# Performance work log

Hardware: AMD Instinct MI355X
Metric: run time of the kernel (lower is better)

Reference implementation:

```python
import jax, jax.numpy as jnp
import numpy as np

NUM_HEADS = 16

def setup_inputs() -> dict:
    key = jax.random.key(0)
    ks = jax.random.split(key, 11)
    B, S, D, H = 2, 2048, 1024, 1024
    s = lambda k, shape, scale=1.0: (jax.random.normal(k, shape, dtype=jnp.float32) * scale)
    return {
        "KEY": s(ks[0], (B, S, D)),
        "VALUE": s(ks[1], (B, S, D)),
        "QUERY": s(ks[2], (B, S, D)),
        "Wk_w": s(ks[3], (H, D), 0.02),
        "Wk_b": s(ks[4], (H,), 0.02),
        "Wq_w": s(ks[5], (H, D), 0.02),
        "Wq_b": s(ks[6], (H,), 0.02),
        "Wv_w": s(ks[7], (H, D), 0.02),
        "Wv_b": s(ks[8], (H,), 0.02),
        "Wo_w": s(ks[9], (H, H), 0.02),
        "Wo_b": s(ks[10], (H,), 0.02),
    }


def _split_heads(x, num_heads):
    # torch: reshape (B, S, dh, nh) then permute(0,3,1,2) -> (B, nh, S, dh)
    B, S, H = x.shape
    dh = H // num_heads
    return x.reshape(B, S, dh, num_heads).transpose(0, 3, 1, 2)


def reference(KEY, VALUE, QUERY, Wk_w, Wk_b, Wq_w, Wq_b, Wv_w, Wv_b, Wo_w, Wo_b):
    nh = NUM_HEADS
    k = _split_heads(KEY @ Wk_w.T + Wk_b, nh)      # [B, nh, Sk, dh]
    q = _split_heads(QUERY @ Wq_w.T + Wq_b, nh)    # [B, nh, Sq, dh]
    v = _split_heads(VALUE @ Wv_w.T + Wv_b, nh)    # [B, nh, Sv, dh]
    dh = q.shape[-1]
    score = jnp.einsum('bhij,bhkj->bhik', k, q) / jnp.sqrt(jnp.asarray(dh, k.dtype))  # [B,nh,Sk,Sq]
    # NOTE: faithful to the source — softmax over dim=1 (the HEAD axis)
    attn = jax.nn.softmax(score, axis=1)
    out = jnp.einsum('bhik,bhij->bhjk', attn, v)   # [B, nh, dh, Sq]
    B = out.shape[0]
    # permute(0,2,1,3) -> [B, dh, nh, Sq]; reshape -> [B, dh*nh, Sq]; transpose -> [B, Sq, H]
    out = out.transpose(0, 2, 1, 3).reshape(B, -1, out.shape[-1]).transpose(0, 2, 1)
    res = out @ Wo_w.T + Wo_b                      # dropout is identity in eval mode
    return res
```

## Files before the change

### kernel.cpp

```cpp
#include <hip/hip_runtime.h>
#include <hip/hip_bf16.h>

typedef __attribute__((ext_vector_type(8))) short s8v;
typedef __attribute__((ext_vector_type(4))) short s4v;
typedef __attribute__((ext_vector_type(4))) float f4v;

#define MFMA32(A,B,C) __builtin_amdgcn_mfma_f32_16x16x32_bf16(A,B,C,0,0,0)
#define MFMA16(A,B,C) __builtin_amdgcn_mfma_f32_16x16x16bf16_1k(A,B,C,0,0,0)

typedef __attribute__((address_space(1))) const void* gas1;
typedef __attribute__((address_space(3))) void* las3;
#define GLDS16(g,l) __builtin_amdgcn_global_load_lds((gas1)(const void*)(g),(las3)(void*)(l),16,0,0)

__device__ __forceinline__ unsigned short f2bf(float f){
  unsigned int u = __float_as_uint(f);
  u += 0x7FFFu + ((u>>16)&1u);
  return (unsigned short)(u>>16);
}
__device__ __forceinline__ float bf2f(unsigned short s){
  return __uint_as_float(((unsigned int)s)<<16);
}
__device__ __forceinline__ s4v pack4(f4v v){
  float2 lo; lo.x=v[0]; lo.y=v[1];
  float2 hi; hi.x=v[2]; hi.y=v[3];
  __hip_bfloat162 a = __float22bfloat162_rn(lo);
  __hip_bfloat162 b = __float22bfloat162_rn(hi);
  union{ s4v s; unsigned int u[2]; } r;
  __builtin_memcpy(&r.u[0], &a, 4);
  __builtin_memcpy(&r.u[1], &b, 4);
  return r.s;
}

#define EXPC 0.18033688011112042f

#define BARRIER() do{                                        \
  asm volatile("s_waitcnt lgkmcnt(0)" ::: "memory");         \
  __builtin_amdgcn_s_barrier();                              \
  asm volatile("" ::: "memory");                             \
}while(0)

__global__ __launch_bounds__(256) void conv_in(
    const float* __restrict__ KEY, const float* __restrict__ QUERY, const float* __restrict__ VALUE,
    const float* __restrict__ Wk, const float* __restrict__ Wq, const float* __restrict__ Wv,
    unsigned short* __restrict__ kb, unsigned short* __restrict__ qb,
    unsigned short* __restrict__ vb, unsigned short* __restrict__ wkb,
    unsigned short* __restrict__ wqb, unsigned short* __restrict__ wvb)
{
  const int z = blockIdx.y;
  const size_t n = (z<3)? (size_t)4194304 : (size_t)1048576;
  size_t idx = ((size_t)blockIdx.x*256 + threadIdx.x)*8;
  if(idx >= n) return;
  const float* s = (z==0)?KEY:(z==1)?QUERY:(z==2)?VALUE:(z==3)?Wk:(z==4)?Wq:Wv;
  unsigned short* d = (z==0)?kb:(z==1)?qb:(z==2)?vb:(z==3)?wkb:(z==4)?wqb:wvb;
  float4 a = *(const float4*)&s[idx];
  float4 b = *(const float4*)&s[idx+4];
  union{ s8v v; s4v h[2]; } r;
  r.h[0]=pack4((f4v){a.x,a.y,a.z,a.w});
  r.h[1]=pack4((f4v){b.x,b.y,b.z,b.w});
  *(s8v*)&d[idx]=r.v;
}

__global__ void pack_wo(const float* __restrict__ wo, unsigned short* __restrict__ wop){
  int idx = blockIdx.x*256 + threadIdx.x;
  if(idx >= 1024*1024) return;
  int o = idx >> 10, r = idx & 1023, h = r >> 6, j = r & 63;
  wop[idx] = f2bf(wo[o*1024 + j*16 + h]);
}

__global__ __launch_bounds__(256) void proj_gemm(
    const unsigned short* __restrict__ kbp, const unsigned short* __restrict__ qbp,
    const unsigned short* __restrict__ vbp,
    const unsigned short* __restrict__ wkb, const unsigned short* __restrict__ wqb,
    const unsigned short* __restrict__ wvb,
    const float* __restrict__ bk, const float* __restrict__ bq, const float* __restrict__ bv,
    unsigned short* __restrict__ kh, unsigned short* __restrict__ qh,
    unsigned short* __restrict__ vt)
{
  __shared__ short As[128*64];
  __shared__ short Bs[128*64];
  const int t = threadIdx.x;
  const int z = blockIdx.z;
  const unsigned short* A; const unsigned short* W; const float* bias;
  if(z==0){A=kbp; W=wkb; bias=bk;}
  else if(z==1){A=qbp; W=wqb; bias=bq;}
  else {A=vbp; W=wvb; bias=bv;}
  const int m0 = blockIdx.x*128, n0 = blockIdx.y*128;
  const int l = t&63, w = t>>6;
  const int wm = (w>>1)*64, wn = (w&1)*64;
  const int row16 = l&15, quad = l>>4;
  f4v acc[4][4];
  #pragma unroll
  for(int i=0;i<4;i++)
    #pragma unroll
    for(int j=0;j<4;j++) acc[i][j] = (f4v){0.f,0.f,0.f,0.f};

  const int sr=t>>3, sc=(t&7)*8;
  for(int k0=0;k0<1024;k0+=64){
    #pragma unroll
    for(int p=0;p<4;p++){
      GLDS16(&A[(size_t)(m0+p*32+sr)*1024 + k0 + sc], &As[(p*32+sr)*64 + sc]);
      GLDS16(&W[(size_t)(n0+p*32+sr)*1024 + k0 + sc], &Bs[(p*32+sr)*64 + sc]);
    }
    __syncthreads();
    #pragma unroll
    for(int kk=0; kk<64; kk+=32){
      s8v af[4], bf[4];
      #pragma unroll
      for(int mt=0;mt<4;mt++) af[mt] = *(const s8v*)&As[(wm+mt*16+row16)*64 + kk + quad*8];
      #pragma unroll
      for(int nt=0;nt<4;nt++) bf[nt] = *(const s8v*)&Bs[(wn+nt*16+row16)*64 + kk + quad*8];
      #pragma unroll
      for(int mt=0;mt<4;mt++)
        #pragma unroll
        for(int nt=0;nt<4;nt++)
          acc[mt][nt] = MFMA32(af[mt], bf[nt], acc[mt][nt]);
    }
    __syncthreads();
  }

  const int jb = (n0+wn)>>4;
  const float bv0 = bias[n0+wn+ 0+row16];
  const float bv1 = bias[n0+wn+16+row16];
  const float bv2 = bias[n0+wn+32+row16];
  const float bv3 = bias[n0+wn+48+row16];
  if(z==2){
    #pragma unroll
    for(int mt=0;mt<4;mt++){
      const int m = m0+wm+mt*16;
      const int bb=m>>11, ss=m&2047, it=ss>>4;
      const size_t base = (((size_t)(bb*16+row16))*128 + it)*64;
      #pragma unroll
      for(int nt=0;nt<4;nt++){
        const float bn = (nt==0)?bv0:(nt==1)?bv1:(nt==2)?bv2:bv3;
        f4v vals = {acc[mt][nt][0]+bn, acc[mt][nt][1]+bn,
                    acc[mt][nt][2]+bn, acc[mt][nt][3]+bn};
        *(s4v*)&vt[(base + jb+nt)*16 + quad*4] = pack4(vals);
      }
    }
  } else {
    unsigned short* dst = (z==0)? kh : qh;
    #pragma unroll
    for(int mt=0;mt<4;mt++){
      #pragma unroll
      for(int r=0;r<4;r++){
        const int m = m0+wm+mt*16+quad*4+r;
        const int bb=m>>11, ss=m&2047;
        f4v vals = {acc[mt][0][r]+bv0, acc[mt][1][r]+bv1,
                    acc[mt][2][r]+bv2, acc[mt][3][r]+bv3};
        *(s4v*)&dst[((size_t)(bb*16+row16)*2048 + ss)*64 + jb] = pack4(vals);
      }
    }
  }
}

__global__ __launch_bounds__(512) void fused_attn(
    const unsigned short* __restrict__ kh, const unsigned short* __restrict__ qh,
    const unsigned short* __restrict__ vt, unsigned short* __restrict__ opart)
{
  __shared__ unsigned short Ks[256*64];
  __shared__ unsigned short Vs[1024*16];
  __shared__ f4v dpart[2][4][64];

  const int t=threadIdx.x, l=t&63, w=t>>6;
  const int qg=w>>2, hg=w&3;
  const int row16=l&15, quad=l>>4;
  const int bid=blockIdx.x;
  const int combo=bid&7, qb=bid>>3;
  const int ih=combo&3, b=combo>>2;
  const int q0=qb*32+qg*16, h0=hg*4;
  const int ibase=ih*512;

  s8v qf[4][2];
  #pragma unroll
  for(int hh=0;hh<4;hh++){
    const unsigned short* qp=&qh[(size_t)((b*16+h0+hh)*2048 + q0+row16)*64];
    qf[hh][0]=*(const s8v*)&qp[quad*8];
    qf[hh][1]=*(const s8v*)&qp[32+quad*8];
  }

  const int ksl=t&7;
  const unsigned short* kp[4]; int kw[4];
  #pragma unroll
  for(int p=0;p<4;p++){
    const int urow=p*64+(t>>3), h=urow>>4, i=urow&15;
    kp[p]=&kh[((size_t)(b*16+h)*2048 + ibase + i)*64 + ksl*8];
    kw[p]=urow*64 + ((ksl^(urow&7))<<3);
  }
  const int half=t&1;
  const int vkey=(t>>3)&3;
  const unsigned short* vp[4]; int vw0[4], vw1[4];
  #pragma unroll
  for(int p=0;p<4;p++){
    const int row=p*256+(t>>1), h=row>>6, j=row&63;
    vp[p]=&vt[((((size_t)(b*16+h))*128 + ih*32)*64 + j)*16 + half*8];
    vw0[p]=row*16 + (((2*half+0)^vkey)<<2);
    vw1[p]=row*16 + (((2*half+1)^vkey)<<2);
  }

  f4v o[4][4];
  #pragma unroll
  for(int i=0;i<4;i++)
    #pragma unroll
    for(int j=0;j<4;j++) o[i][j]=(f4v){0.f,0.f,0.f,0.f};

  s8v kreg[4], vtmp[4];
  #pragma unroll
  for(int p=0;p<4;p++) kreg[p]=*(const s8v*)(kp[p]);
  #pragma unroll
  for(int p=0;p<4;p++) vtmp[p]=*(const s8v*)(vp[p]);
  #pragma unroll
  for(int p=0;p<4;p++) *(s8v*)&Ks[kw[p]] = kreg[p];
  #pragma unroll
  for(int p=0;p<4;p++) kreg[p]=*(const s8v*)(kp[p] + 1024);
  BARRIER();

  const int sw0=(quad^(row16&7))<<3, sw1=((quad+4)^(row16&7))<<3;
  const int vsw=(quad^((row16>>2)&3))<<2;

  #pragma unroll 1
  for(int it=0; it<32; ++it){
    #pragma unroll
    for(int p=0;p<4;p++){
      s4v lo={vtmp[p][0],vtmp[p][1],vtmp[p][2],vtmp[p][3]};
      s4v hi={vtmp[p][4],vtmp[p][5],vtmp[p][6],vtmp[p][7]};
      *(s4v*)&Vs[vw0[p]]=lo;
      *(s4v*)&Vs[vw1[p]]=hi;
    }
    const int tv=((it+1)&31)*1024;
    #pragma unroll
    for(int p=0;p<4;p++) vtmp[p]=*(const s8v*)(vp[p]+tv);
    f4v e0[4];
    #pragma unroll
    for(int hh=0;hh<4;hh++){
      const unsigned short* kb=&Ks[((h0+hh)*16+row16)*64];
      f4v S={0.f,0.f,0.f,0.f};
      S=MFMA32(*(const s8v*)&kb[sw0], qf[hh][0], S);
      S=MFMA32(*(const s8v*)&kb[sw1], qf[hh][1], S);
      #pragma unroll
      for(int r=0;r<4;r++) e0[hh][r]=__builtin_amdgcn_exp2f(S[r]*EXPC);
    }
    f4v d0=(e0[0]+e0[1])+(e0[2]+e0[3]);
    dpart[qg][hg][l]=d0;
    BARRIER();
    f4v s0=(dpart[qg][0][l]+dpart[qg][1][l])+(dpart[qg][2][l]+dpart[qg][3][l]);
    f4v r0;
    #pragma unroll
    for(int r=0;r<4;r++) r0[r]=__builtin_amdgcn_rcpf(s0[r]);
    #pragma unroll
    for(int p=0;p<4;p++) *(s8v*)&Ks[kw[p]] = kreg[p];
    const int tk=((it+2)&31)*1024;
    #pragma unroll
    for(int p=0;p<4;p++) kreg[p]=*(const s8v*)(kp[p]+tk);
    s4v p0[4];
    #pragma unroll
    for(int hh=0;hh<4;hh++) p0[hh]=pack4(e0[hh]*r0);
    #pragma unroll
    for(int hh=0;hh<4;hh++){
      #pragma unroll
      for(int jt=0;jt<4;jt++){
        const int vrow=((h0+hh)*64+jt*16+row16)*16;
        s4v v0=*(const s4v*)&Vs[vrow + vsw];
        o[hh][jt]=MFMA16(v0, p0[hh], o[hh][jt]);
      }
    }
    BARRIER();
  }

  #pragma unroll
  for(int hh=0;hh<4;hh++)
    #pragma unroll
    for(int jt=0;jt<4;jt++)
      *(s4v*)&opart[(size_t)((ih*2+b)*2048 + q0+row16)*1024 + (h0+hh)*64 + jt*16 + quad*4]
        = pack4(o[hh][jt]);
}

__global__ __launch_bounds__(256) void reduce_o(
    const unsigned short* __restrict__ op, unsigned short* __restrict__ out2)
{
  size_t e = ((size_t)blockIdx.x*256 + threadIdx.x)*8;
  s8v a = *(const s8v*)&op[e];
  s8v b = *(const s8v*)&op[(size_t)4194304 + e];
  s8v c = *(const s8v*)&op[(size_t)2*4194304 + e];
  s8v d = *(const s8v*)&op[(size_t)3*4194304 + e];
  f4v lo, hi;
  #pragma unroll
  for(int i=0;i<4;i++)
    lo[i] = (bf2f((unsigned short)a[i])+bf2f((unsigned short)b[i]))
          + (bf2f((unsigned short)c[i])+bf2f((unsigned short)d[i]));
  #pragma unroll
  for(int i=0;i<4;i++)
    hi[i] = (bf2f((unsigned short)a[i+4])+bf2f((unsigned short)b[i+4]))
          + (bf2f((unsigned short)c[i+4])+bf2f((unsigned short)d[i+4]));
  *(s4v*)&out2[e]   = pack4(lo);
  *(s4v*)&out2[e+4] = pack4(hi);
}

__global__ __launch_bounds__(256) void out_gemm(
    const unsigned short* __restrict__ A, const unsigned short* __restrict__ Bm,
    const float* __restrict__ bias, float* __restrict__ out)
{
  __shared__ short As[128*64];
  __shared__ short Bs[128*64];
  const int t=threadIdx.x, l=t&63, w=t>>6;
  const int row16=l&15, quad=l>>4;
  const int m0=blockIdx.x*128, n0=blockIdx.y*128;
  const int wm=(w>>1)*64, wn=(w&1)*64;
  f4v acc[4][4];
  #pragma unroll
  for(int i=0;i<4;i++)
    #pragma unroll
    for(int j=0;j<4;j++) acc[i][j] = (f4v){0.f,0.f,0.f,0.f};

  const int sr=t>>3, sc=(t&7)*8;
  for(int k0=0;k0<1024;k0+=64){
    #pragma unroll
    for(int p=0;p<4;p++){
      GLDS16(&A [(size_t)(m0+p*32+sr)*1024 + k0 + sc], &As[(p*32+sr)*64 + sc]);
      GLDS16(&Bm[(size_t)(n0+p*32+sr)*1024 + k0 + sc], &Bs[(p*32+sr)*64 + sc]);
    }
    __syncthreads();
    #pragma unroll
    for(int kk=0; kk<64; kk+=32){
      s8v af[4], bf[4];
      #pragma unroll
      for(int mt=0;mt<4;mt++) af[mt] = *(const s8v*)&As[(wm+mt*16+row16)*64 + kk + quad*8];
      #pragma unroll
      for(int nt=0;nt<4;nt++) bf[nt] = *(const s8v*)&Bs[(wn+nt*16+row16)*64 + kk + quad*8];
      #pragma unroll
      for(int mt=0;mt<4;mt++)
        #pragma unroll
        for(int nt=0;nt<4;nt++)
          acc[mt][nt] = MFMA32(af[mt], bf[nt], acc[mt][nt]);
    }
    __syncthreads();
  }
  #pragma unroll
  for(int nt=0;nt<4;nt++){
    const int n = n0+wn+nt*16+row16;
    const float bias_n = bias[n];
    #pragma unroll
    for(int mt=0;mt<4;mt++)
      #pragma unroll
      for(int r=0;r<4;r++){
        const int m = m0+wm+mt*16+quad*4+r;
        out[(size_t)m*1024 + n] = acc[mt][nt][r] + bias_n;
      }
  }
}

extern "C" void kernel_launch(void* const* d_in, const int* in_sizes, int n_in,
                              void* d_out, int out_size, void* d_ws, size_t ws_size,
                              hipStream_t stream)
{
  const float* KEY   = (const float*)d_in[0];
  const float* VALUE = (const float*)d_in[1];
  const float* QUERY = (const float*)d_in[2];
  const float* Wk = (const float*)d_in[3];
  const float* bk = (const float*)d_in[4];
  const float* Wq = (const float*)d_in[5];
  const float* bq = (const float*)d_in[6];
  const float* Wv = (const float*)d_in[7];
  const float* bv = (const float*)d_in[8];
  const float* Wo = (const float*)d_in[9];
  const float* bo = (const float*)d_in[10];

  char* ws = (char*)d_ws;
  unsigned short* kb   = (unsigned short*)(ws);
  unsigned short* qb   = (unsigned short*)(ws +  8388608);
  unsigned short* vb   = (unsigned short*)(ws + 16777216);
  unsigned short* wkb  = (unsigned short*)(ws + 25165824);
  unsigned short* wqb  = (unsigned short*)(ws + 27262976);
  unsigned short* wvb  = (unsigned short*)(ws + 29360128);
  unsigned short* kh   = (unsigned short*)(ws + 33554432);
  unsigned short* qh   = (unsigned short*)(ws + 41943040);
  unsigned short* vt   = (unsigned short*)(ws + 50331648);
  unsigned short* opart= (unsigned short*)(ws);
  unsigned short* wop  = (unsigned short*)(ws + 33554432);
  unsigned short* out2 = (unsigned short*)(ws + 35651584);

  conv_in   <<<dim3(2048,6), dim3(256), 0, stream>>>(KEY,QUERY,VALUE,Wk,Wq,Wv,kb,qb,vb,wkb,wqb,wvb);
  proj_gemm <<<dim3(32,8,3), dim3(256), 0, stream>>>(kb,qb,vb,wkb,wqb,wvb,bk,bq,bv,kh,qh,vt);
  fused_attn<<<dim3(512),    dim3(512), 0, stream>>>(kh,qh,vt,opart);
  pack_wo   <<<dim3(4096),   dim3(256), 0, stream>>>(Wo,wop);
  reduce_o  <<<dim3(2048),   dim3(256), 0, stream>>>(opart,out2);
  out_gemm  <<<dim3(32,8),   dim3(256), 0, stream>>>(out2,wop,bo,(float*)d_out);
}
```

Measured before the change: 303.9 us.

## Load attention K/V fragments directly from global and coalesce Wo packing

The fused attention kernel no longer stages K and V tiles through shared memory. Each lane now loads its MFMA operand fragments straight from global memory into registers, prefetching the next K fragment one iteration ahead. The per-iteration trailing barrier is replaced by a double-buffered denominator array, so only one barrier per iteration remains. The pack_wo kernel now reads float4 and transposes through shared memory for vectorized writes, trading cooperative coalesced staging in attention for more, smaller uncoalesced global loads that rely on cache.

```diff
diff --git a/kernel.cpp b/kernel.cpp
--- a/kernel.cpp
+++ b/kernel.cpp
@@ -60,11 +60,24 @@
   *(s8v*)&d[idx]=r.v;
 }
 
-__global__ void pack_wo(const float* __restrict__ wo, unsigned short* __restrict__ wop){
-  int idx = blockIdx.x*256 + threadIdx.x;
-  if(idx >= 1024*1024) return;
-  int o = idx >> 10, r = idx & 1023, h = r >> 6, j = r & 63;
-  wop[idx] = f2bf(wo[o*1024 + j*16 + h]);
+__global__ __launch_bounds__(256) void pack_wo(const float* __restrict__ wo,
+                                              unsigned short* __restrict__ wop){
+  __shared__ unsigned short tile[4][1024];
+  const int o0 = blockIdx.x*4;
+  const int t = threadIdx.x;
+  const int r = t>>6, u = t&63;
+  #pragma unroll
+  for(int e4=0;e4<4;e4++){
+    float4 v = *(const float4*)&wo[(size_t)(o0+r)*1024 + u*16 + e4*4];
+    tile[r][(e4*4+0)*64 + u] = f2bf(v.x);
+    tile[r][(e4*4+1)*64 + u] = f2bf(v.y);
+    tile[r][(e4*4+2)*64 + u] = f2bf(v.z);
+    tile[r][(e4*4+3)*64 + u] = f2bf(v.w);
+  }
+  __syncthreads();
+  const unsigned short* flat = &tile[0][0];
+  *(s8v*)&wop[(size_t)o0*1024 + t*16]     = *(const s8v*)&flat[t*16];
+  *(s8v*)&wop[(size_t)o0*1024 + t*16 + 8] = *(const s8v*)&flat[t*16 + 8];
 }
 
 __global__ __launch_bounds__(256) void proj_gemm(
@@ -157,9 +170,7 @@
     const unsigned short* __restrict__ kh, const unsigned short* __restrict__ qh,
     const unsigned short* __restrict__ vt, unsigned short* __restrict__ opart)
 {
-  __shared__ unsigned short Ks[256*64];
-  __shared__ unsigned short Vs[1024*16];
-  __shared__ f4v dpart[2][4][64];
+  __shared__ f4v dpart[2][2][4][64];
 
   const int t=threadIdx.x, l=t&63, w=t>>6;
   const int qg=w>>2, hg=w&3;
@@ -178,24 +189,8 @@
     qf[hh][1]=*(const s8v*)&qp[32+quad*8];
   }
 
-  const int ksl=t&7;
-  const unsigned short* kp[4]; int kw[4];
-  #pragma unroll
-  for(int p=0;p<4;p++){
-    const int urow=p*64+(t>>3), h=urow>>4, i=urow&15;
-    kp[p]=&kh[((size_t)(b*16+h)*2048 + ibase + i)*64 + ksl*8];
-    kw[p]=urow*64 + ((ksl^(urow&7))<<3);
-  }
-  const int half=t&1;
-  const int vkey=(t>>3)&3;
-  const unsigned short* vp[4]; int vw0[4], vw1[4];
-  #pragma unroll
-  for(int p=0;p<4;p++){
-    const int row=p*256+(t>>1), h=row>>6, j=row&63;
-    vp[p]=&vt[((((size_t)(b*16+h))*128 + ih*32)*64 + j)*16 + half*8];
-    vw0[p]=row*16 + (((2*half+0)^vkey)<<2);
-    vw1[p]=row*16 + (((2*half+1)^vkey)<<2);
-  }
+  const unsigned short* kbase=&kh[((size_t)(b*16+h0)*2048 + ibase + row16)*64 + quad*8];
+  const unsigned short* vbase=&vt[((((size_t)(b*16+h0))*128 + ih*32)*64 + row16)*16 + quad*4];
 
   f4v o[4][4];
   #pragma unroll
@@ -203,67 +198,54 @@
     #pragma unroll
     for(int j=0;j<4;j++) o[i][j]=(f4v){0.f,0.f,0.f,0.f};
 
-  s8v kreg[4], vtmp[4];
-  #pragma unroll
-  for(int p=0;p<4;p++) kreg[p]=*(const s8v*)(kp[p]);
-  #pragma unroll
-  for(int p=0;p<4;p++) vtmp[p]=*(const s8v*)(vp[p]);
-  #pragma unroll
-  for(int p=0;p<4;p++) *(s8v*)&Ks[kw[p]] = kreg[p];
-  #pragma unroll
-  for(int p=0;p<4;p++) kreg[p]=*(const s8v*)(kp[p] + 1024);
-  BARRIER();
-
-  const int sw0=(quad^(row16&7))<<3, sw1=((quad+4)^(row16&7))<<3;
-  const int vsw=(quad^((row16>>2)&3))<<2;
+  s8v kf[4][2];
+  #pragma unroll
+  for(int hh=0;hh<4;hh++){
+    kf[hh][0]=*(const s8v*)(kbase + hh*131072);
+    kf[hh][1]=*(const s8v*)(kbase + hh*131072 + 32);
+  }
 
   #pragma unroll 1
   for(int it=0; it<32; ++it){
-    #pragma unroll
-    for(int p=0;p<4;p++){
-      s4v lo={vtmp[p][0],vtmp[p][1],vtmp[p][2],vtmp[p][3]};
-      s4v hi={vtmp[p][4],vtmp[p][5],vtmp[p][6],vtmp[p][7]};
-      *(s4v*)&Vs[vw0[p]]=lo;
-      *(s4v*)&Vs[vw1[p]]=hi;
-    }
-    const int tv=((it+1)&31)*1024;
-    #pragma unroll
-    for(int p=0;p<4;p++) vtmp[p]=*(const s8v*)(vp[p]+tv);
+    const int par=it&1;
+    const int off=it*1024;
+    s4v vf[4][4];
+    #pragma unroll
+    for(int hh=0;hh<4;hh++)
+      #pragma unroll
+      for(int jt=0;jt<4;jt++)
+        vf[hh][jt]=*(const s4v*)(vbase + off + hh*131072 + jt*256);
     f4v e0[4];
     #pragma unroll
     for(int hh=0;hh<4;hh++){
-      const unsigned short* kb=&Ks[((h0+hh)*16+row16)*64];
       f4v S={0.f,0.f,0.f,0.f};
-      S=MFMA32(*(const s8v*)&kb[sw0], qf[hh][0], S);
-      S=MFMA32(*(const s8v*)&kb[sw1], qf[hh][1], S);
+      S=MFMA32(kf[hh][0], qf[hh][0], S);
+      S=MFMA32(kf[hh][1], qf[hh][1], S);
       #pragma unroll
       for(int r=0;r<4;r++) e0[hh][r]=__builtin_amdgcn_exp2f(S[r]*EXPC);
     }
+    const int offn=((it+1)&31)*1024;
+    #pragma unroll
+    for(int hh=0;hh<4;hh++){
+      kf[hh][0]=*(const s8v*)(kbase + offn + hh*131072);
+      kf[hh][1]=*(const s8v*)(kbase + offn + hh*131072 + 32);
+    }
     f4v d0=(e0[0]+e0[1])+(e0[2]+e0[3]);
-    dpart[qg][hg][l]=d0;
+    dpart[par][qg][hg][l]=d0;
     BARRIER();
-    f4v s0=(dpart[qg][0][l]+dpart[qg][1][l])+(dpart[qg][2][l]+dpart[qg][3][l]);
+    f4v s0=(dpart[par][qg][0][l]+dpart[par][qg][1][l])
+          +(dpart[par][qg][2][l]+dpart[par][qg][3][l]);
     f4v r0;
     #pragma unroll
     for(int r=0;r<4;r++) r0[r]=__builtin_amdgcn_rcpf(s0[r]);
-    #pragma unroll
-    for(int p=0;p<4;p++) *(s8v*)&Ks[kw[p]] = kreg[p];
-    const int tk=((it+2)&31)*1024;
-    #pragma unroll
-    for(int p=0;p<4;p++) kreg[p]=*(const s8v*)(kp[p]+tk);
     s4v p0[4];
     #pragma unroll
     for(int hh=0;hh<4;hh++) p0[hh]=pack4(e0[hh]*r0);
     #pragma unroll
-    for(int hh=0;hh<4;hh++){
-      #pragma unroll
-      for(int jt=0;jt<4;jt++){
-        const int vrow=((h0+hh)*64+jt*16+row16)*16;
-        s4v v0=*(const s4v*)&Vs[vrow + vsw];
-        o[hh][jt]=MFMA16(v0, p0[hh], o[hh][jt]);
-      }
-    }
-    BARRIER();
+    for(int hh=0;hh<4;hh++)
+      #pragma unroll
+      for(int jt=0;jt<4;jt++)
+        o[hh][jt]=MFMA16(vf[hh][jt], p0[hh], o[hh][jt]);
   }
 
   #pragma unroll
@@ -381,7 +363,7 @@
   conv_in   <<<dim3(2048,6), dim3(256), 0, stream>>>(KEY,QUERY,VALUE,Wk,Wq,Wv,kb,qb,vb,wkb,wqb,wvb);
   proj_gemm <<<dim3(32,8,3), dim3(256), 0, stream>>>(kb,qb,vb,wkb,wqb,wvb,bk,bq,bv,kh,qh,vt);
   fused_attn<<<dim3(512),    dim3(512), 0, stream>>>(kh,qh,vt,opart);
-  pack_wo   <<<dim3(4096),   dim3(256), 0, stream>>>(Wo,wop);
+  pack_wo   <<<dim3(256),    dim3(256), 0, stream>>>(Wo,wop);
   reduce_o  <<<dim3(2048),   dim3(256), 0, stream>>>(opart,out2);
   out_gemm  <<<dim3(32,8),   dim3(256), 0, stream>>>(out2,wop,bo,(float*)d_out);
 }
```

Measured after the change: 393.0 us. +29.3%, slower.

## Fuse partial-output reduction into output GEMM and coalesce Wo packing

Applied to the files above, without the earlier changes.

Removes the separate reduce_o kernel. The output GEMM now loads the four bf16 partial outputs, sums them in fp32 and writes the packed tile into shared memory itself, in place of the async global-to-LDS copy. pack_wo is rewritten to read float4 rows, transpose through shared memory and store 16-byte vectors, so its global accesses are coalesced. A small tweak reuses the wave's own denominator partial in attention. This saves a kernel launch and the intermediate round trip, but every out_gemm block (across the n dimension) now re-reads and re-sums the A partials through synchronous loads.

```diff
diff --git a/kernel.cpp b/kernel.cpp
--- a/kernel.cpp
+++ b/kernel.cpp
@@ -60,11 +60,24 @@
   *(s8v*)&d[idx]=r.v;
 }
 
-__global__ void pack_wo(const float* __restrict__ wo, unsigned short* __restrict__ wop){
-  int idx = blockIdx.x*256 + threadIdx.x;
-  if(idx >= 1024*1024) return;
-  int o = idx >> 10, r = idx & 1023, h = r >> 6, j = r & 63;
-  wop[idx] = f2bf(wo[o*1024 + j*16 + h]);
+__global__ __launch_bounds__(256) void pack_wo(const float* __restrict__ wo,
+                                              unsigned short* __restrict__ wop){
+  __shared__ unsigned short tile[4][1024];
+  const int o0 = blockIdx.x*4;
+  const int t = threadIdx.x;
+  const int r = t>>6, u = t&63;
+  #pragma unroll
+  for(int e4=0;e4<4;e4++){
+    float4 v = *(const float4*)&wo[(size_t)(o0+r)*1024 + u*16 + e4*4];
+    tile[r][(e4*4+0)*64 + u] = f2bf(v.x);
+    tile[r][(e4*4+1)*64 + u] = f2bf(v.y);
+    tile[r][(e4*4+2)*64 + u] = f2bf(v.z);
+    tile[r][(e4*4+3)*64 + u] = f2bf(v.w);
+  }
+  __syncthreads();
+  const unsigned short* flat = &tile[0][0];
+  *(s8v*)&wop[(size_t)o0*1024 + t*16]     = *(const s8v*)&flat[t*16];
+  *(s8v*)&wop[(size_t)o0*1024 + t*16 + 8] = *(const s8v*)&flat[t*16 + 8];
 }
 
 __global__ __launch_bounds__(256) void proj_gemm(
@@ -242,7 +255,9 @@
     f4v d0=(e0[0]+e0[1])+(e0[2]+e0[3]);
     dpart[qg][hg][l]=d0;
     BARRIER();
-    f4v s0=(dpart[qg][0][l]+dpart[qg][1][l])+(dpart[qg][2][l]+dpart[qg][3][l]);
+    f4v s0 = d0;
+    #pragma unroll
+    for(int g=0; g<4; ++g) if(g!=hg) s0 += dpart[qg][g][l];
     f4v r0;
     #pragma unroll
     for(int r=0;r<4;r++) r0[r]=__builtin_amdgcn_rcpf(s0[r]);
@@ -258,8 +273,8 @@
     for(int hh=0;hh<4;hh++){
       #pragma unroll
       for(int jt=0;jt<4;jt++){
-        const int vrow=((h0+hh)*64+jt*16+row16)*16;
-        s4v v0=*(const s4v*)&Vs[vrow + vsw];
+        const int vrow=(h0+hh)*64+jt*16+row16;
+        s4v v0=*(const s4v*)&Vs[vrow*16 + vsw];
         o[hh][jt]=MFMA16(v0, p0[hh], o[hh][jt]);
       }
     }
@@ -274,29 +289,8 @@
         = pack4(o[hh][jt]);
 }
 
-__global__ __launch_bounds__(256) void reduce_o(
-    const unsigned short* __restrict__ op, unsigned short* __restrict__ out2)
-{
-  size_t e = ((size_t)blockIdx.x*256 + threadIdx.x)*8;
-  s8v a = *(const s8v*)&op[e];
-  s8v b = *(const s8v*)&op[(size_t)4194304 + e];
-  s8v c = *(const s8v*)&op[(size_t)2*4194304 + e];
-  s8v d = *(const s8v*)&op[(size_t)3*4194304 + e];
-  f4v lo, hi;
-  #pragma unroll
-  for(int i=0;i<4;i++)
-    lo[i] = (bf2f((unsigned short)a[i])+bf2f((unsigned short)b[i]))
-          + (bf2f((unsigned short)c[i])+bf2f((unsigned short)d[i]));
-  #pragma unroll
-  for(int i=0;i<4;i++)
-    hi[i] = (bf2f((unsigned short)a[i+4])+bf2f((unsigned short)b[i+4]))
-          + (bf2f((unsigned short)c[i+4])+bf2f((unsigned short)d[i+4]));
-  *(s4v*)&out2[e]   = pack4(lo);
-  *(s4v*)&out2[e+4] = pack4(hi);
-}
-
 __global__ __launch_bounds__(256) void out_gemm(
-    const unsigned short* __restrict__ A, const unsigned short* __restrict__ Bm,
+    const unsigned short* __restrict__ op, const unsigned short* __restrict__ Bm,
     const float* __restrict__ bias, float* __restrict__ out)
 {
   __shared__ short As[128*64];
@@ -315,7 +309,22 @@
   for(int k0=0;k0<1024;k0+=64){
     #pragma unroll
     for(int p=0;p<4;p++){
-      GLDS16(&A [(size_t)(m0+p*32+sr)*1024 + k0 + sc], &As[(p*32+sr)*64 + sc]);
+      const size_t e = (size_t)(m0+p*32+sr)*1024 + k0 + sc;
+      s8v a0 = *(const s8v*)&op[e];
+      s8v a1 = *(const s8v*)&op[e + (size_t)4194304];
+      s8v a2 = *(const s8v*)&op[e + (size_t)8388608];
+      s8v a3 = *(const s8v*)&op[e + (size_t)12582912];
+      f4v lo, hi;
+      #pragma unroll
+      for(int i=0;i<4;i++){
+        lo[i] = (bf2f((unsigned short)a0[i])+bf2f((unsigned short)a1[i]))
+              + (bf2f((unsigned short)a2[i])+bf2f((unsigned short)a3[i]));
+        hi[i] = (bf2f((unsigned short)a0[i+4])+bf2f((unsigned short)a1[i+4]))
+              + (bf2f((unsigned short)a2[i+4])+bf2f((unsigned short)a3[i+4]));
+      }
+      union{ s8v v; s4v h[2]; } rr;
+      rr.h[0]=pack4(lo); rr.h[1]=pack4(hi);
+      *(s8v*)&As[(p*32+sr)*64 + sc] = rr.v;
       GLDS16(&Bm[(size_t)(n0+p*32+sr)*1024 + k0 + sc], &Bs[(p*32+sr)*64 + sc]);
     }
     __syncthreads();
@@ -376,12 +385,10 @@
   unsigned short* vt   = (unsigned short*)(ws + 50331648);
   unsigned short* opart= (unsigned short*)(ws);
   unsigned short* wop  = (unsigned short*)(ws + 33554432);
-  unsigned short* out2 = (unsigned short*)(ws + 35651584);
 
   conv_in   <<<dim3(2048,6), dim3(256), 0, stream>>>(KEY,QUERY,VALUE,Wk,Wq,Wv,kb,qb,vb,wkb,wqb,wvb);
   proj_gemm <<<dim3(32,8,3), dim3(256), 0, stream>>>(kb,qb,vb,wkb,wqb,wvb,bk,bq,bv,kh,qh,vt);
   fused_attn<<<dim3(512),    dim3(512), 0, stream>>>(kh,qh,vt,opart);
-  pack_wo   <<<dim3(4096),   dim3(256), 0, stream>>>(Wo,wop);
-  reduce_o  <<<dim3(2048),   dim3(256), 0, stream>>>(opart,out2);
-  out_gemm  <<<dim3(32,8),   dim3(256), 0, stream>>>(out2,wop,bo,(float*)d_out);
-}
+  pack_wo   <<<dim3(256),    dim3(256), 0, stream>>>(Wo,wop);
+  out_gemm  <<<dim3(32,8),   dim3(256), 0, stream>>>(opart,wop,bo,(float*)d_out);
+}
```

New measurement: 322.7 us. 1.06x slower.

## Halve attention block query tile and coalesce Wo packing via shared-memory transpose

Applied to the files above, without the earlier changes.

The fused attention kernel now uses 256-thread blocks covering 16 queries instead of 512 threads covering 32. The grid doubles to 1024 blocks, and each thread loads twice as many K/V chunks into shared memory. K/V tiles are therefore reused across fewer queries, which doubles global/LDS staging traffic per query in exchange for more, smaller blocks and fewer waves per barrier. Separately, pack_wo is rewritten to read Wo with float4 loads, transpose through shared memory, and write 16-byte chunks, replacing strided scalar gathers.

```diff
diff --git a/kernel.cpp b/kernel.cpp
--- a/kernel.cpp
+++ b/kernel.cpp
@@ -60,11 +60,24 @@
   *(s8v*)&d[idx]=r.v;
 }
 
-__global__ void pack_wo(const float* __restrict__ wo, unsigned short* __restrict__ wop){
-  int idx = blockIdx.x*256 + threadIdx.x;
-  if(idx >= 1024*1024) return;
-  int o = idx >> 10, r = idx & 1023, h = r >> 6, j = r & 63;
-  wop[idx] = f2bf(wo[o*1024 + j*16 + h]);
+__global__ __launch_bounds__(256) void pack_wo(const float* __restrict__ wo,
+                                              unsigned short* __restrict__ wop){
+  __shared__ unsigned short tile[4][1024];
+  const int o0 = blockIdx.x*4;
+  const int t = threadIdx.x;
+  const int r = t>>6, u = t&63;
+  #pragma unroll
+  for(int e4=0;e4<4;e4++){
+    float4 v = *(const float4*)&wo[(size_t)(o0+r)*1024 + u*16 + e4*4];
+    tile[r][(e4*4+0)*64 + u] = f2bf(v.x);
+    tile[r][(e4*4+1)*64 + u] = f2bf(v.y);
+    tile[r][(e4*4+2)*64 + u] = f2bf(v.z);
+    tile[r][(e4*4+3)*64 + u] = f2bf(v.w);
+  }
+  __syncthreads();
+  const unsigned short* flat = &tile[0][0];
+  *(s8v*)&wop[(size_t)o0*1024 + t*16]     = *(const s8v*)&flat[t*16];
+  *(s8v*)&wop[(size_t)o0*1024 + t*16 + 8] = *(const s8v*)&flat[t*16 + 8];
 }
 
 __global__ __launch_bounds__(256) void proj_gemm(
@@ -153,21 +166,21 @@
   }
 }
 
-__global__ __launch_bounds__(512) void fused_attn(
+__global__ __launch_bounds__(256) void fused_attn(
     const unsigned short* __restrict__ kh, const unsigned short* __restrict__ qh,
     const unsigned short* __restrict__ vt, unsigned short* __restrict__ opart)
 {
   __shared__ unsigned short Ks[256*64];
   __shared__ unsigned short Vs[1024*16];
-  __shared__ f4v dpart[2][4][64];
+  __shared__ f4v dpart[4][64];
 
   const int t=threadIdx.x, l=t&63, w=t>>6;
-  const int qg=w>>2, hg=w&3;
+  const int hg=w;
   const int row16=l&15, quad=l>>4;
   const int bid=blockIdx.x;
   const int combo=bid&7, qb=bid>>3;
   const int ih=combo&3, b=combo>>2;
-  const int q0=qb*32+qg*16, h0=hg*4;
+  const int q0=qb*16, h0=hg*4;
   const int ibase=ih*512;
 
   s8v qf[4][2];
@@ -179,19 +192,19 @@
   }
 
   const int ksl=t&7;
-  const unsigned short* kp[4]; int kw[4];
-  #pragma unroll
-  for(int p=0;p<4;p++){
-    const int urow=p*64+(t>>3), h=urow>>4, i=urow&15;
+  const unsigned short* kp[8]; int kw[8];
+  #pragma unroll
+  for(int p=0;p<8;p++){
+    const int urow=p*32+(t>>3), h=urow>>4, i=urow&15;
     kp[p]=&kh[((size_t)(b*16+h)*2048 + ibase + i)*64 + ksl*8];
     kw[p]=urow*64 + ((ksl^(urow&7))<<3);
   }
   const int half=t&1;
   const int vkey=(t>>3)&3;
-  const unsigned short* vp[4]; int vw0[4], vw1[4];
-  #pragma unroll
-  for(int p=0;p<4;p++){
-    const int row=p*256+(t>>1), h=row>>6, j=row&63;
+  const unsigned short* vp[8]; int vw0[8], vw1[8];
+  #pragma unroll
+  for(int p=0;p<8;p++){
+    const int row=p*128+(t>>1), h=row>>6, j=row&63;
     vp[p]=&vt[((((size_t)(b*16+h))*128 + ih*32)*64 + j)*16 + half*8];
     vw0[p]=row*16 + (((2*half+0)^vkey)<<2);
     vw1[p]=row*16 + (((2*half+1)^vkey)<<2);
@@ -203,15 +216,15 @@
     #pragma unroll
     for(int j=0;j<4;j++) o[i][j]=(f4v){0.f,0.f,0.f,0.f};
 
-  s8v kreg[4], vtmp[4];
-  #pragma unroll
-  for(int p=0;p<4;p++) kreg[p]=*(const s8v*)(kp[p]);
-  #pragma unroll
-  for(int p=0;p<4;p++) vtmp[p]=*(const s8v*)(vp[p]);
-  #pragma unroll
-  for(int p=0;p<4;p++) *(s8v*)&Ks[kw[p]] = kreg[p];
-  #pragma unroll
-  for(int p=0;p<4;p++) kreg[p]=*(const s8v*)(kp[p] + 1024);
+  s8v kreg[8], vtmp[8];
+  #pragma unroll
+  for(int p=0;p<8;p++) kreg[p]=*(const s8v*)(kp[p]);
+  #pragma unroll
+  for(int p=0;p<8;p++) vtmp[p]=*(const s8v*)(vp[p]);
+  #pragma unroll
+  for(int p=0;p<8;p++) *(s8v*)&Ks[kw[p]] = kreg[p];
+  #pragma unroll
+  for(int p=0;p<8;p++) kreg[p]=*(const s8v*)(kp[p] + 1024);
   BARRIER();
 
   const int sw0=(quad^(row16&7))<<3, sw1=((quad+4)^(row16&7))<<3;
@@ -220,7 +233,7 @@
   #pragma unroll 1
   for(int it=0; it<32; ++it){
     #pragma unroll
-    for(int p=0;p<4;p++){
+    for(int p=0;p<8;p++){
       s4v lo={vtmp[p][0],vtmp[p][1],vtmp[p][2],vtmp[p][3]};
       s4v hi={vtmp[p][4],vtmp[p][5],vtmp[p][6],vtmp[p][7]};
       *(s4v*)&Vs[vw0[p]]=lo;
@@ -228,7 +241,7 @@
     }
     const int tv=((it+1)&31)*1024;
     #pragma unroll
-    for(int p=0;p<4;p++) vtmp[p]=*(const s8v*)(vp[p]+tv);
+    for(int p=0;p<8;p++) vtmp[p]=*(const s8v*)(vp[p]+tv);
     f4v e0[4];
     #pragma unroll
     for(int hh=0;hh<4;hh++){
@@ -240,17 +253,19 @@
       for(int r=0;r<4;r++) e0[hh][r]=__builtin_amdgcn_exp2f(S[r]*EXPC);
     }
     f4v d0=(e0[0]+e0[1])+(e0[2]+e0[3]);
-    dpart[qg][hg][l]=d0;
+    dpart[hg][l]=d0;
     BARRIER();
-    f4v s0=(dpart[qg][0][l]+dpart[qg][1][l])+(dpart[qg][2][l]+dpart[qg][3][l]);
+    f4v s0 = d0;
+    #pragma unroll
+    for(int g=0; g<4; ++g) if(g!=hg) s0 += dpart[g][l];
     f4v r0;
     #pragma unroll
     for(int r=0;r<4;r++) r0[r]=__builtin_amdgcn_rcpf(s0[r]);
     #pragma unroll
-    for(int p=0;p<4;p++) *(s8v*)&Ks[kw[p]] = kreg[p];
+    for(int p=0;p<8;p++) *(s8v*)&Ks[kw[p]] = kreg[p];
     const int tk=((it+2)&31)*1024;
     #pragma unroll
-    for(int p=0;p<4;p++) kreg[p]=*(const s8v*)(kp[p]+tk);
+    for(int p=0;p<8;p++) kreg[p]=*(const s8v*)(kp[p]+tk);
     s4v p0[4];
     #pragma unroll
     for(int hh=0;hh<4;hh++) p0[hh]=pack4(e0[hh]*r0);
@@ -258,8 +273,8 @@
     for(int hh=0;hh<4;hh++){
       #pragma unroll
       for(int jt=0;jt<4;jt++){
-        const int vrow=((h0+hh)*64+jt*16+row16)*16;
-        s4v v0=*(const s4v*)&Vs[vrow + vsw];
+        const int vrow=(h0+hh)*64+jt*16+row16;
+        s4v v0=*(const s4v*)&Vs[vrow*16 + vsw];
         o[hh][jt]=MFMA16(v0, p0[hh], o[hh][jt]);
       }
     }
@@ -380,8 +395,8 @@
 
   conv_in   <<<dim3(2048,6), dim3(256), 0, stream>>>(KEY,QUERY,VALUE,Wk,Wq,Wv,kb,qb,vb,wkb,wqb,wvb);
   proj_gemm <<<dim3(32,8,3), dim3(256), 0, stream>>>(kb,qb,vb,wkb,wqb,wvb,bk,bq,bv,kh,qh,vt);
-  fused_attn<<<dim3(512),    dim3(512), 0, stream>>>(kh,qh,vt,opart);
-  pack_wo   <<<dim3(4096),   dim3(256), 0, stream>>>(Wo,wop);
+  fused_attn<<<dim3(1024),   dim3(256), 0, stream>>>(kh,qh,vt,opart);
+  pack_wo   <<<dim3(256),    dim3(256), 0, stream>>>(Wo,wop);
   reduce_o  <<<dim3(2048),   dim3(256), 0, stream>>>(opart,out2);
   out_gemm  <<<dim3(32,8),   dim3(256), 0, stream>>>(out2,wop,bo,(float*)d_out);
 }
```

Result: slower. 394.7 us (+29.9%).
